# Kernel optimization log

Measured on AMD Instinct MI355X. Metric: run time of the kernel, lower is better.

Reference implementation:

```python
import jax, jax.numpy as jnp
import numpy as np

B, S, D = 64, 512, 768


def setup_inputs() -> dict:
    key = jax.random.key(0)
    x = jax.random.normal(key, (B, S, D), dtype=jnp.float32)
    rng = np.random.default_rng(0)
    b0 = rng.integers(0, S // 4, size=B)          # aspect start
    alen = rng.integers(1, 6, size=B)             # aspect length in [1,5]
    b1 = b0 + alen - 1                            # aspect end (inclusive)
    tlen = rng.integers(b1 + 1, S + 1)            # text length in (b1, S]
    return {
        "x": x,
        "aspect_boundary_indices": jnp.asarray(np.stack([b0, b1], axis=1), dtype=jnp.int32),
        "text_len": jnp.asarray(tlen, dtype=jnp.int32),
        "aspect_len": jnp.asarray(alen, dtype=jnp.int32),
    }


def _prox_mat(aspect_boundary_indices, text_len, aspect_len, seq_len):
    # Vectorized version of the per-sample/per-position numpy loops.
    j = jnp.arange(seq_len, dtype=jnp.float32)[None, :]                # [1,S]
    b0 = aspect_boundary_indices[:, 0:1].astype(jnp.float32)          # [B,1]
    b1 = aspect_boundary_indices[:, 1:2].astype(jnp.float32)          # [B,1]
    tl = text_len[:, None].astype(jnp.float32)                        # [B,1]
    ctx = (text_len - aspect_len)[:, None].astype(jnp.float32)        # [B,1]
    left = 1.0 - (b0 - j) / ctx          # j < b0
    mid = 1.0 / ctx                      # b0 <= j <= b1
    right = 1.0 - (j - b1) / ctx         # b1 < j < text_len
    prox = jnp.where(j < b0, left, jnp.where(j <= b1, mid, right))
    prox = jnp.where(j < tl, prox, 0.0)  # padding positions -> 0
    return jnp.clip(prox, 0.0, 1.0)      # valid bernoulli probabilities


def reference(x, aspect_boundary_indices, text_len, aspect_len):
    seq_len = x.shape[1]
    prox = _prox_mat(aspect_boundary_indices, text_len, aspect_len, seq_len)  # [B,S]
    mask = jax.random.bernoulli(jax.random.key(42), prox).astype(jnp.float32)
    scale = mask / (prox + 1e-5)                                              # [B,S]
    return scale[:, :, None] * x
```

## Files before the change

### kernel.cpp

```cpp
#include <hip/hip_runtime.h>


static constexpr int Bn = 64, Sn = 512, Dn = 768;
static constexpr int ROWS = Bn * Sn;
static constexpr int TOT4 = Bn * Sn * Dn / 4;

__device__ __forceinline__ unsigned rotl32(unsigned x, int d) {
  return (x << d) | (x >> (32 - d));
}

__device__ __forceinline__ void threefry2x32_0_42(unsigned x0, unsigned x1,
                                                  unsigned& o0, unsigned& o1) {
  const unsigned ks0 = 0u;
  const unsigned ks1 = 42u;
  const unsigned ks2 = 0u ^ 42u ^ 0x1BD11BDAu;
  unsigned v0 = x0 + ks0;
  unsigned v1 = x1 + ks1;
#define RG(a, b, c, d)                       \
  v0 += v1; v1 = rotl32(v1, a); v1 ^= v0;    \
  v0 += v1; v1 = rotl32(v1, b); v1 ^= v0;    \
  v0 += v1; v1 = rotl32(v1, c); v1 ^= v0;    \
  v0 += v1; v1 = rotl32(v1, d); v1 ^= v0;
  RG(13, 15, 26, 6)   v0 += ks1; v1 += ks2 + 1u;
  RG(17, 29, 16, 24)  v0 += ks2; v1 += ks0 + 2u;
  RG(13, 15, 26, 6)   v0 += ks0; v1 += ks1 + 3u;
  RG(17, 29, 16, 24)  v0 += ks1; v1 += ks2 + 4u;
  RG(13, 15, 26, 6)   v0 += ks2; v1 += ks0 + 5u;
#undef RG
  o0 = v0;
  o1 = v1;
}

__device__ __forceinline__ float row_scale(int row, unsigned bits,
                                           const int* __restrict__ abi,
                                           const int* __restrict__ tl,
                                           const int* __restrict__ al) {
  int b = row >> 9;
  int s = row & (Sn - 1);
  float jf  = (float)s;
  float b0f = (float)abi[2 * b];
  float b1f = (float)abi[2 * b + 1];
  int   tli = tl[b];
  float tlf = (float)tli;
  float ctx = (float)(tli - al[b]);

  float prox;
  if (jf < b0f)       prox = 1.0f - (b0f - jf) / ctx;
  else if (jf <= b1f) prox = 1.0f / ctx;
  else                prox = 1.0f - (jf - b1f) / ctx;
  prox = (jf < tlf) ? prox : 0.0f;
  prox = fminf(fmaxf(prox, 0.0f), 1.0f);

  float u = __uint_as_float((bits >> 9) | 0x3f800000u) - 1.0f;
  float mask = (u < prox) ? 1.0f : 0.0f;
  return mask / (prox + 1e-5f);
}

__global__ void scale_kernel(const int* __restrict__ abi,
                             const int* __restrict__ tl,
                             const int* __restrict__ al,
                             float* __restrict__ scale) {
  int i = blockIdx.x * blockDim.x + threadIdx.x;
  if (i >= ROWS) return;
  unsigned o0, o1;
  threefry2x32_0_42(0u, (unsigned)i, o0, o1);
  unsigned bits = o0 ^ o1;
  scale[i] = row_scale(i, bits, abi, tl, al);
}

__global__ void apply_kernel(const float4* __restrict__ x,
                             const float* __restrict__ scale,
                             float4* __restrict__ out) {
  int i = blockIdx.x * blockDim.x + threadIdx.x;
  if (i >= TOT4) return;
  unsigned row = (unsigned)i / 192u;
  float s = scale[row];
  float4 v = x[i];
  v.x *= s; v.y *= s; v.z *= s; v.w *= s;
  out[i] = v;
}

__global__ void fused_kernel(const float4* __restrict__ x,
                             const int* __restrict__ abi,
                             const int* __restrict__ tl,
                             const int* __restrict__ al,
                             float4* __restrict__ out) {
  int row = blockIdx.x;
  int t   = threadIdx.x;
  unsigned o0, o1;
  threefry2x32_0_42(0u, (unsigned)row, o0, o1);
  unsigned bits = o0 ^ o1;
  float s = row_scale(row, bits, abi, tl, al);
  int e = row * (Dn / 4) + t;
  float4 v = x[e];
  v.x *= s; v.y *= s; v.z *= s; v.w *= s;
  out[e] = v;
}

extern "C" void kernel_launch(void* const* d_in, const int* in_sizes, int n_in,
                              void* d_out, int out_size, void* d_ws, size_t ws_size,
                              hipStream_t stream) {
  const float* x  = (const float*)d_in[0];
  const int* abi  = (const int*)d_in[1];
  const int* tl   = (const int*)d_in[2];
  const int* al   = (const int*)d_in[3];
  float* out = (float*)d_out;

  if (ws_size >= (size_t)ROWS * sizeof(float)) {
    float* scale = (float*)d_ws;
    scale_kernel<<<ROWS / 256, 256, 0, stream>>>(abi, tl, al, scale);
    apply_kernel<<<TOT4 / 256, 256, 0, stream>>>((const float4*)x, scale,
                                                 (float4*)out);
  } else {
    fused_kernel<<<ROWS, Dn / 4, 0, stream>>>((const float4*)x, abi, tl, al,
                                              (float4*)out);
  }
}
```

Before: 179.0 us.

## Fuse scale and apply into one kernel with one wavefront per row

Replaces the two-kernel path (scale precompute into workspace, then apply) with a single fused kernel. Each 64-lane wavefront handles one row, computes the threefry-based scale redundantly per lane, and processes three float4 loads per lane. This removes a kernel launch and the scale buffer round trip, and raises per-thread memory-level parallelism. The cost is redundant RNG computation in every lane.

```diff
diff --git a/kernel.cpp b/kernel.cpp
--- a/kernel.cpp
+++ b/kernel.cpp
@@ -3,7 +3,7 @@
 
 static constexpr int Bn = 64, Sn = 512, Dn = 768;
 static constexpr int ROWS = Bn * Sn;
-static constexpr int TOT4 = Bn * Sn * Dn / 4;
+static constexpr int F4_PER_ROW = Dn / 4;
 
 __device__ __forceinline__ unsigned rotl32(unsigned x, int d) {
   return (x << d) | (x >> (32 - d));
@@ -31,10 +31,14 @@
   o1 = v1;
 }
 
-__device__ __forceinline__ float row_scale(int row, unsigned bits,
+__device__ __forceinline__ float row_scale(int row,
                                            const int* __restrict__ abi,
                                            const int* __restrict__ tl,
                                            const int* __restrict__ al) {
+  unsigned o0, o1;
+  threefry2x32_0_42(0u, (unsigned)row, o0, o1);
+  unsigned bits = o0 ^ o1;
+
   int b = row >> 9;
   int s = row & (Sn - 1);
   float jf  = (float)s;
@@ -56,45 +60,28 @@
   return mask / (prox + 1e-5f);
 }
 
-__global__ void scale_kernel(const int* __restrict__ abi,
-                             const int* __restrict__ tl,
-                             const int* __restrict__ al,
-                             float* __restrict__ scale) {
-  int i = blockIdx.x * blockDim.x + threadIdx.x;
-  if (i >= ROWS) return;
-  unsigned o0, o1;
-  threefry2x32_0_42(0u, (unsigned)i, o0, o1);
-  unsigned bits = o0 ^ o1;
-  scale[i] = row_scale(i, bits, abi, tl, al);
-}
+__global__ void __launch_bounds__(256)
+pos_dropout_fused(const float4* __restrict__ x,
+                  const int* __restrict__ abi,
+                  const int* __restrict__ tl,
+                  const int* __restrict__ al,
+                  float4* __restrict__ out) {
+  int gtid = blockIdx.x * 256 + threadIdx.x;
+  int row  = gtid >> 6;
+  int lane = gtid & 63;
 
-__global__ void apply_kernel(const float4* __restrict__ x,
-                             const float* __restrict__ scale,
-                             float4* __restrict__ out) {
-  int i = blockIdx.x * blockDim.x + threadIdx.x;
-  if (i >= TOT4) return;
-  unsigned row = (unsigned)i / 192u;
-  float s = scale[row];
-  float4 v = x[i];
-  v.x *= s; v.y *= s; v.z *= s; v.w *= s;
-  out[i] = v;
-}
+  float s = row_scale(row, abi, tl, al);
 
-__global__ void fused_kernel(const float4* __restrict__ x,
-                             const int* __restrict__ abi,
-                             const int* __restrict__ tl,
-                             const int* __restrict__ al,
-                             float4* __restrict__ out) {
-  int row = blockIdx.x;
-  int t   = threadIdx.x;
-  unsigned o0, o1;
-  threefry2x32_0_42(0u, (unsigned)row, o0, o1);
-  unsigned bits = o0 ^ o1;
-  float s = row_scale(row, bits, abi, tl, al);
-  int e = row * (Dn / 4) + t;
-  float4 v = x[e];
-  v.x *= s; v.y *= s; v.z *= s; v.w *= s;
-  out[e] = v;
+  int base = row * F4_PER_ROW + lane;
+  float4 v0 = x[base];
+  float4 v1 = x[base + 64];
+  float4 v2 = x[base + 128];
+  v0.x *= s; v0.y *= s; v0.z *= s; v0.w *= s;
+  v1.x *= s; v1.y *= s; v1.z *= s; v1.w *= s;
+  v2.x *= s; v2.y *= s; v2.z *= s; v2.w *= s;
+  out[base]       = v0;
+  out[base + 64]  = v1;
+  out[base + 128] = v2;
 }
 
 extern "C" void kernel_launch(void* const* d_in, const int* in_sizes, int n_in,
@@ -106,13 +93,6 @@
   const int* al   = (const int*)d_in[3];
   float* out = (float*)d_out;
 
-  if (ws_size >= (size_t)ROWS * sizeof(float)) {
-    float* scale = (float*)d_ws;
-    scale_kernel<<<ROWS / 256, 256, 0, stream>>>(abi, tl, al, scale);
-    apply_kernel<<<TOT4 / 256, 256, 0, stream>>>((const float4*)x, scale,
-                                                 (float4*)out);
-  } else {
-    fused_kernel<<<ROWS, Dn / 4, 0, stream>>>((const float4*)x, abi, tl, al,
-                                              (float4*)out);
-  }
+  pos_dropout_fused<<<ROWS / 4, 256, 0, stream>>>(
+      (const float4*)x, abi, tl, al, (float4*)out);
 }
```

Result: no change. 179.9 us (+0.5%).
